# Performance work log

Measured on AMD Instinct MI355X. Metric: run time of the kernel, lower is better.

The kernel has to match this reference:

```python
import jax, jax.numpy as jnp
import numpy as np

N_ATOM, N_BOND, N_MOL, D = 250000, 250000, 10000, 64
BN_EPS = 1e-5


def _bn(x, gamma, beta):
    # torch BatchNorm1d training-mode math (biased variance)
    m = jnp.mean(x, axis=0)
    v = jnp.var(x, axis=0)
    return (x - m) * jax.lax.rsqrt(v + BN_EPS) * gamma + beta


def setup_inputs() -> dict:
    key = jax.random.key(0)
    ks = jax.random.split(key, 12)
    h = jax.random.normal(ks[0], (N_ATOM, D), jnp.float32)
    e = jax.random.normal(ks[1], (N_BOND, D), jnp.float32)
    u = jax.random.normal(ks[2], (N_MOL, D), jnp.float32)
    norm_atom = jax.random.uniform(ks[3], (N_ATOM, 1), jnp.float32)
    norm_bond = jax.random.uniform(ks[4], (N_BOND, 1), jnp.float32)
    bond_u = jax.random.randint(ks[5], (N_BOND,), 0, N_ATOM, jnp.int32)
    bond_v = jax.random.randint(ks[6], (N_BOND,), 0, N_ATOM, jnp.int32)
    atom2mol = jax.random.randint(ks[7], (N_ATOM,), 0, N_MOL, jnp.int32)
    bond2mol = jax.random.randint(ks[8], (N_BOND,), 0, N_MOL, jnp.int32)
    # 9 Linear layers A..I stacked: order A,B,C,D,E,F,G,H,I
    Ws = jax.random.normal(ks[9], (9, D, D), jnp.float32) * 0.05
    bs = jax.random.normal(ks[10], (9, D), jnp.float32) * 0.05
    bn_gamma = jnp.ones((3, D), jnp.float32)   # [e, h, u]
    bn_beta = jnp.zeros((3, D), jnp.float32)
    return dict(h=h, e=e, u=u, norm_atom=norm_atom, norm_bond=norm_bond,
                Ws=Ws, bs=bs, bn_gamma=bn_gamma, bn_beta=bn_beta,
                bond_u=bond_u, bond_v=bond_v, atom2mol=atom2mol, bond2mol=bond2mol)


def reference(h, e, u, norm_atom, norm_bond, Ws, bs, bn_gamma, bn_beta,
              bond_u, bond_v, atom2mol, bond2mol):
    lin = lambda x, i: x @ Ws[i] + bs[i]
    Ah, Dh, Eh = lin(h, 0), lin(h, 3), lin(h, 4)
    Be = lin(e, 1)
    Cu, Fu = lin(u, 2), lin(u, 5)

    # bond update: a2b (sum of Ah of both endpoints) + b2b self-loop + g2b broadcast
    e_new = Ah[bond_u] + Ah[bond_v] + Be + Cu[bond2mol]
    e_new = e_new * norm_bond                  # graph_norm
    e_new = _bn(e_new, bn_gamma[0], bn_beta[0])
    e_new = jax.nn.elu(e_new)

    # atom update: a2a self-loop + gated b2a (select_not_equal == other endpoint's Eh) + g2a
    sig = jax.nn.sigmoid(e_new)                # [N_BOND, D]
    dst = jnp.concatenate([bond_u, bond_v])    # each bond sends to both endpoints
    Eh_other = jnp.concatenate([Eh[bond_v], Eh[bond_u]])
    sig2 = jnp.concatenate([sig, sig])
    num = jax.ops.segment_sum(sig2 * Eh_other, dst, num_segments=N_ATOM)
    den = jax.ops.segment_sum(sig2, dst, num_segments=N_ATOM) + 1e-6
    h_new = Dh + num / den + Fu[atom2mol]
    h_new = h_new * norm_atom                  # graph_norm
    h_new = _bn(h_new, bn_gamma[1], bn_beta[1])
    h_new = jax.nn.elu(h_new)

    # global update: mean(Gh over atoms) + mean(He over bonds) + g2g self-loop Iu
    Gh, He, Iu = lin(h_new, 6), lin(e_new, 7), lin(u, 8)
    cnt_a = jax.ops.segment_sum(jnp.ones((N_ATOM, 1), h.dtype), atom2mol, num_segments=N_MOL)
    cnt_b = jax.ops.segment_sum(jnp.ones((N_BOND, 1), e.dtype), bond2mol, num_segments=N_MOL)
    u_new = (jax.ops.segment_sum(Gh, atom2mol, num_segments=N_MOL) / jnp.maximum(cnt_a, 1.0)
             + jax.ops.segment_sum(He, bond2mol, num_segments=N_MOL) / jnp.maximum(cnt_b, 1.0)
             + Iu)
    u_new = _bn(u_new, bn_gamma[2], bn_beta[2])
    u_new = jax.nn.elu(u_new)

    return h_new, e_new, u_new
```

## Files before the change

### kernel.cpp

```cpp
#include <hip/hip_runtime.h>
#include <cmath>

#define DD 64
#define TILE 64
#define BLK 256

__device__ __forceinline__ float elu_f(float x) {
  return x > 0.f ? x : expm1f(x);
}

__device__ __forceinline__ void fma4(float4& a, float s, const float4 b) {
  a.x = fmaf(s, b.x, a.x);
  a.y = fmaf(s, b.y, a.y);
  a.z = fmaf(s, b.z, a.z);
  a.w = fmaf(s, b.w, a.w);
}
__device__ __forceinline__ void add4(float4& a, const float4 b) {
  a.x += b.x; a.y += b.y; a.z += b.z; a.w += b.w;
}
__device__ __forceinline__ void sqacc4(float4& a, const float4 b) {
  a.x = fmaf(b.x, b.x, a.x);
  a.y = fmaf(b.y, b.y, a.y);
  a.z = fmaf(b.z, b.z, a.z);
  a.w = fmaf(b.w, b.w, a.w);
}
__device__ __forceinline__ void scale4(float4& a, float s) {
  a.x *= s; a.y *= s; a.z *= s; a.w *= s;
}

__device__ __forceinline__ void matmul_tile(const float (*xs)[DD + 4], const float (*wl)[DD],
                                            int r0, int c0, float4 acc[4]) {
#pragma unroll 2
  for (int k0 = 0; k0 < DD; k0 += 4) {
    float4 x0 = *(const float4*)&xs[r0 + 0][k0];
    float4 x1 = *(const float4*)&xs[r0 + 1][k0];
    float4 x2 = *(const float4*)&xs[r0 + 2][k0];
    float4 x3 = *(const float4*)&xs[r0 + 3][k0];
    float4 w0 = *(const float4*)&wl[k0 + 0][c0];
    float4 w1 = *(const float4*)&wl[k0 + 1][c0];
    float4 w2 = *(const float4*)&wl[k0 + 2][c0];
    float4 w3 = *(const float4*)&wl[k0 + 3][c0];
    fma4(acc[0], x0.x, w0); fma4(acc[0], x0.y, w1); fma4(acc[0], x0.z, w2); fma4(acc[0], x0.w, w3);
    fma4(acc[1], x1.x, w0); fma4(acc[1], x1.y, w1); fma4(acc[1], x1.z, w2); fma4(acc[1], x1.w, w3);
    fma4(acc[2], x2.x, w0); fma4(acc[2], x2.y, w1); fma4(acc[2], x2.z, w2); fma4(acc[2], x2.w, w3);
    fma4(acc[3], x3.x, w0); fma4(acc[3], x3.y, w1); fma4(acc[3], x3.z, w2); fma4(acc[3], x3.w, w3);
  }
}

__global__ void cnt_kernel(const int* __restrict__ a2m, int na,
                           const int* __restrict__ b2m, int nb,
                           const int* __restrict__ bu, const int* __restrict__ bv,
                           int* __restrict__ cnta_i, int* __restrict__ cntb_i,
                           int* __restrict__ deg) {
  int i = blockIdx.x * blockDim.x + threadIdx.x;
  if (i < na) {
    atomicAdd(&cnta_i[a2m[i]], 1);
  } else if (i < na + nb) {
    int b = i - na;
    atomicAdd(&cntb_i[b2m[b]], 1);
    atomicAdd(&deg[bu[b]], 1);
    atomicAdd(&deg[bv[b]], 1);
  }
}

__global__ void seg_alloc_kernel(const int* __restrict__ deg, int n,
                                 int* __restrict__ start, int* __restrict__ gcount) {
  int i = blockIdx.x * blockDim.x + threadIdx.x;
  int lane = threadIdx.x & 63;
  int d = (i < n) ? deg[i] : 0;
  int pre = d;
#pragma unroll
  for (int off = 1; off < 64; off <<= 1) {
    int t = __shfl_up(pre, off, 64);
    if (lane >= off) pre += t;
  }
  int total = __shfl(pre, 63, 64);
  int excl = pre - d;
  int base = 0;
  if (lane == 63) base = atomicAdd(gcount, total);
  base = __shfl(base, 63, 64);
  if (i < n) start[i] = base + excl;
}

__global__ void fill_kernel(const int* __restrict__ bu, const int* __restrict__ bv, int nb,
                            const int* __restrict__ start, int* __restrict__ cur,
                            int2* __restrict__ adj) {
  int b = blockIdx.x * blockDim.x + threadIdx.x;
  if (b < nb) {
    int a0 = bu[b], a1 = bv[b];
    int p = start[a0] + atomicAdd(&cur[a0], 1);
    adj[p] = make_int2(b, a1);
    int q = start[a1] + atomicAdd(&cur[a1], 1);
    adj[q] = make_int2(b, a0);
  }
}

__global__ void fill_mol_kernel(const int* __restrict__ a2m, int na,
                                const int* __restrict__ b2m, int nb,
                                const int* __restrict__ start_ma, int* __restrict__ cur_ma,
                                int* __restrict__ lista,
                                const int* __restrict__ start_mb, int* __restrict__ cur_mb,
                                int* __restrict__ listb) {
  int i = blockIdx.x * blockDim.x + threadIdx.x;
  if (i < na) {
    int m = a2m[i];
    lista[start_ma[m] + atomicAdd(&cur_ma[m], 1)] = i;
  } else if (i < na + nb) {
    int b = i - na;
    int m = b2m[b];
    listb[start_mb[m] + atomicAdd(&cur_mb[m], 1)] = b;
  }
}

__global__ __launch_bounds__(BLK) void lin2_kernel(
    const float* __restrict__ x, int nrows,
    const float* __restrict__ W0, const float* __restrict__ b0, float* __restrict__ out0,
    const float* __restrict__ W1, const float* __restrict__ b1, float* __restrict__ out1) {
  __shared__ __align__(16) float xs[TILE][DD + 4];
  __shared__ __align__(16) float w0[DD][DD];
  __shared__ __align__(16) float w1[DD][DD];
  const int tid = threadIdx.x;
  const int base = blockIdx.x * TILE;
  int rows = nrows - base; if (rows > TILE) rows = TILE;
  for (int l = tid; l < DD * DD; l += BLK) {
    int r = l >> 6, c = l & 63;
    xs[r][c] = (r < rows) ? x[(size_t)(base + r) * DD + c] : 0.f;
    w0[r][c] = W0[l];
    w1[r][c] = W1[l];
  }
  __syncthreads();
  const int tr = tid >> 4, tc = tid & 15;
  const int r0 = tr * 4, c0 = tc * 4;
  float4 accA[4], accB[4];
#pragma unroll
  for (int i = 0; i < 4; ++i) {
    accA[i] = make_float4(0.f, 0.f, 0.f, 0.f);
    accB[i] = make_float4(0.f, 0.f, 0.f, 0.f);
  }
#pragma unroll 1
  for (int k0 = 0; k0 < DD; k0 += 4) {
    float4 x0 = *(const float4*)&xs[r0 + 0][k0];
    float4 x1 = *(const float4*)&xs[r0 + 1][k0];
    float4 x2 = *(const float4*)&xs[r0 + 2][k0];
    float4 x3 = *(const float4*)&xs[r0 + 3][k0];
    float4 wa0 = *(const float4*)&w0[k0 + 0][c0];
    float4 wa1 = *(const float4*)&w0[k0 + 1][c0];
    float4 wa2 = *(const float4*)&w0[k0 + 2][c0];
    float4 wa3 = *(const float4*)&w0[k0 + 3][c0];
    float4 wb0 = *(const float4*)&w1[k0 + 0][c0];
    float4 wb1 = *(const float4*)&w1[k0 + 1][c0];
    float4 wb2 = *(const float4*)&w1[k0 + 2][c0];
    float4 wb3 = *(const float4*)&w1[k0 + 3][c0];
    fma4(accA[0], x0.x, wa0); fma4(accA[0], x0.y, wa1); fma4(accA[0], x0.z, wa2); fma4(accA[0], x0.w, wa3);
    fma4(accA[1], x1.x, wa0); fma4(accA[1], x1.y, wa1); fma4(accA[1], x1.z, wa2); fma4(accA[1], x1.w, wa3);
    fma4(accA[2], x2.x, wa0); fma4(accA[2], x2.y, wa1); fma4(accA[2], x2.z, wa2); fma4(accA[2], x2.w, wa3);
    fma4(accA[3], x3.x, wa0); fma4(accA[3], x3.y, wa1); fma4(accA[3], x3.z, wa2); fma4(accA[3], x3.w, wa3);
    fma4(accB[0], x0.x, wb0); fma4(accB[0], x0.y, wb1); fma4(accB[0], x0.z, wb2); fma4(accB[0], x0.w, wb3);
    fma4(accB[1], x1.x, wb0); fma4(accB[1], x1.y, wb1); fma4(accB[1], x1.z, wb2); fma4(accB[1], x1.w, wb3);
    fma4(accB[2], x2.x, wb0); fma4(accB[2], x2.y, wb1); fma4(accB[2], x2.z, wb2); fma4(accB[2], x2.w, wb3);
    fma4(accB[3], x3.x, wb0); fma4(accB[3], x3.y, wb1); fma4(accB[3], x3.z, wb2); fma4(accB[3], x3.w, wb3);
  }
  float4 bv0 = *(const float4*)&b0[c0];
  float4 bv1 = *(const float4*)&b1[c0];
#pragma unroll
  for (int i = 0; i < 4; ++i) {
    if (r0 + i < rows) {
      size_t rb = (size_t)(base + r0 + i) * DD + c0;
      float4 o0 = accA[i]; add4(o0, bv0);
      float4 o1 = accB[i]; add4(o1, bv1);
      *(float4*)&out0[rb] = o0;
      *(float4*)&out1[rb] = o1;
    }
  }
}

__global__ __launch_bounds__(BLK) void bond1_kernel(
    const float* __restrict__ e, int nrows, int ntiles,
    const float* __restrict__ W1, const float* __restrict__ b1,
    const float* __restrict__ Ah, const float* __restrict__ Cu,
    const int* __restrict__ bu, const int* __restrict__ bv, const int* __restrict__ b2m,
    const float* __restrict__ nrm,
    float* __restrict__ e_pre,
    float* __restrict__ ssum, float* __restrict__ ssq) {
  __shared__ __align__(16) float xs[TILE][DD + 4];
  __shared__ __align__(16) float wl[DD][DD];
  __shared__ int sbu[TILE], sbv[TILE], sbm[TILE];
  __shared__ float snb[TILE];
  __shared__ __align__(16) float red[16][DD];
  const int tid = threadIdx.x;
  const int tr = tid >> 4, tc = tid & 15, r0 = tr * 4, c0 = tc * 4;
  for (int l = tid; l < DD * DD; l += BLK) wl[l >> 6][l & 63] = W1[l];
  float4 bp = *(const float4*)&b1[c0];
  float4 lsum = make_float4(0.f, 0.f, 0.f, 0.f);
  float4 lsq  = make_float4(0.f, 0.f, 0.f, 0.f);
  for (int tile = blockIdx.x; tile < ntiles; tile += gridDim.x) {
    const int base = tile * TILE;
    int rows = nrows - base; if (rows > TILE) rows = TILE;
    __syncthreads();
    for (int l = tid; l < TILE * DD; l += BLK) {
      int r = l >> 6, c = l & 63;
      xs[r][c] = (r < rows) ? e[(size_t)(base + r) * DD + c] : 0.f;
    }
    if (tid < TILE) {
      bool v = tid < rows;
      int rb = base + tid;
      sbu[tid] = v ? bu[rb] : 0;
      sbv[tid] = v ? bv[rb] : 0;
      sbm[tid] = v ? b2m[rb] : 0;
      snb[tid] = v ? nrm[rb] : 0.f;
    }
    __syncthreads();
    float4 acc[4];
#pragma unroll
    for (int i = 0; i < 4; ++i) acc[i] = make_float4(0.f, 0.f, 0.f, 0.f);
    matmul_tile(xs, wl, r0, c0, acc);
#pragma unroll
    for (int i = 0; i < 4; ++i) {
      int r = r0 + i;
      if (r < rows) {
        int rb = base + r;
        float nb = snb[r];
        float4 ga = *(const float4*)&Ah[(size_t)sbu[r] * DD + c0];
        float4 gb = *(const float4*)&Ah[(size_t)sbv[r] * DD + c0];
        float4 gc = *(const float4*)&Cu[(size_t)sbm[r] * DD + c0];
        float4 o = acc[i];
        add4(o, bp); add4(o, ga); add4(o, gb); add4(o, gc);
        scale4(o, nb);
        add4(lsum, o); sqacc4(lsq, o);
        *(float4*)&e_pre[(size_t)rb * DD + c0] = o;
      }
    }
  }
  __syncthreads();
  *(float4*)&red[tr][c0] = lsum;
  __syncthreads();
  if (tid < DD) {
    float s = 0.f;
#pragma unroll
    for (int t = 0; t < 16; ++t) s += red[t][tid];
    atomicAdd(&ssum[tid], s);
  }
  __syncthreads();
  *(float4*)&red[tr][c0] = lsq;
  __syncthreads();
  if (tid < DD) {
    float s = 0.f;
#pragma unroll
    for (int t = 0; t < 16; ++t) s += red[t][tid];
    atomicAdd(&ssq[tid], s);
  }
}

__global__ void bnfinal_kernel(const float* __restrict__ ssum, const float* __restrict__ ssq,
                               const float* __restrict__ gamma, const float* __restrict__ beta,
                               float invN, float* __restrict__ scale, float* __restrict__ shift) {
  int j = threadIdx.x;
  float m = ssum[j] * invN;
  float v = ssq[j] * invN - m * m;
  float sc = gamma[j] * rsqrtf(v + 1e-5f);
  scale[j] = sc;
  shift[j] = beta[j] - m * sc;
}

__global__ void bn_elu_vec_kernel(float* __restrict__ x, long n4,
                                  const float* __restrict__ scale,
                                  const float* __restrict__ shift) {
  long stride = (long)gridDim.x * blockDim.x;
  for (long i = blockIdx.x * (long)blockDim.x + threadIdx.x; i < n4; i += stride) {
    float4 v = ((float4*)x)[i];
    int c0 = (int)((i & 15) << 2);
    float4 sc = *(const float4*)&scale[c0];
    float4 sh = *(const float4*)&shift[c0];
    v.x = elu_f(fmaf(v.x, sc.x, sh.x));
    v.y = elu_f(fmaf(v.y, sc.y, sh.y));
    v.z = elu_f(fmaf(v.z, sc.z, sh.z));
    v.w = elu_f(fmaf(v.w, sc.w, sh.w));
    ((float4*)x)[i] = v;
  }
}

__global__ __launch_bounds__(BLK) void agg_kernel(
    const float* __restrict__ e_act, const float* __restrict__ Eh,
    const int* __restrict__ start, const int* __restrict__ deg,
    const int2* __restrict__ adj, int na,
    float* __restrict__ aggout) {
  int wid = (int)((blockIdx.x * (unsigned)blockDim.x + threadIdx.x) >> 6);
  int lane = threadIdx.x & 63;
  if (wid >= na) return;
  int s = start[wid], d = deg[wid];
  float num = 0.f, den = 0.f;
  for (int k = 0; k < d; ++k) {
    int2 ent = adj[s + k];
    float ev = e_act[(size_t)ent.x * DD + lane];
    float sg = 1.f / (1.f + expf(-ev));
    float eh = Eh[(size_t)ent.y * DD + lane];
    num = fmaf(sg, eh, num);
    den += sg;
  }
  aggout[(size_t)wid * DD + lane] = num / (den + 1e-6f);
}

__global__ __launch_bounds__(BLK) void molsum_kernel(
    const float* __restrict__ src, const int* __restrict__ start,
    const int* __restrict__ cnt, const int* __restrict__ list, int nm,
    float* __restrict__ out) {
  int wid = (int)((blockIdx.x * (unsigned)blockDim.x + threadIdx.x) >> 6);
  int lane = threadIdx.x & 63;
  if (wid >= nm) return;
  int s = start[wid], c = cnt[wid];
  float acc = 0.f;
  for (int k = 0; k < c; ++k) {
    acc += src[(size_t)list[s + k] * DD + lane];
  }
  out[(size_t)wid * DD + lane] = acc;
}

__global__ __launch_bounds__(BLK) void atom1_kernel(
    const float* __restrict__ h, int nrows, int ntiles,
    const float* __restrict__ W3, const float* __restrict__ b3,
    const float* __restrict__ Fu,
    const int* __restrict__ a2m, const float* __restrict__ nrm,
    float* __restrict__ hio,
    float* __restrict__ ssum, float* __restrict__ ssq) {
  __shared__ __align__(16) float xs[TILE][DD + 4];
  __shared__ __align__(16) float wl[DD][DD];
  __shared__ int sam[TILE];
  __shared__ float sna[TILE];
  __shared__ __align__(16) float red[16][DD];
  const int tid = threadIdx.x;
  const int tr = tid >> 4, tc = tid & 15, r0 = tr * 4, c0 = tc * 4;
  for (int l = tid; l < DD * DD; l += BLK) wl[l >> 6][l & 63] = W3[l];
  float4 bp = *(const float4*)&b3[c0];
  float4 lsum = make_float4(0.f, 0.f, 0.f, 0.f);
  float4 lsq  = make_float4(0.f, 0.f, 0.f, 0.f);
  for (int tile = blockIdx.x; tile < ntiles; tile += gridDim.x) {
    const int base = tile * TILE;
    int rows = nrows - base; if (rows > TILE) rows = TILE;
    __syncthreads();
    for (int l = tid; l < TILE * DD; l += BLK) {
      int r = l >> 6, c = l & 63;
      xs[r][c] = (r < rows) ? h[(size_t)(base + r) * DD + c] : 0.f;
    }
    if (tid < TILE) {
      bool v = tid < rows;
      int rb = base + tid;
      sam[tid] = v ? a2m[rb] : 0;
      sna[tid] = v ? nrm[rb] : 0.f;
    }
    __syncthreads();
    float4 acc[4];
#pragma unroll
    for (int i = 0; i < 4; ++i) acc[i] = make_float4(0.f, 0.f, 0.f, 0.f);
    matmul_tile(xs, wl, r0, c0, acc);
#pragma unroll
    for (int i = 0; i < 4; ++i) {
      int r = r0 + i;
      if (r < rows) {
        size_t rb = (size_t)(base + r) * DD + c0;
        float na = sna[r];
        float4 g4 = *(const float4*)&hio[rb];
        float4 f4 = *(const float4*)&Fu[(size_t)sam[r] * DD + c0];
        float4 o;
        o.x = (acc[i].x + bp.x + g4.x + f4.x) * na;
        o.y = (acc[i].y + bp.y + g4.y + f4.y) * na;
        o.z = (acc[i].z + bp.z + g4.z + f4.z) * na;
        o.w = (acc[i].w + bp.w + g4.w + f4.w) * na;
        add4(lsum, o); sqacc4(lsq, o);
        *(float4*)&hio[rb] = o;
      }
    }
  }
  __syncthreads();
  *(float4*)&red[tr][c0] = lsum;
  __syncthreads();
  if (tid < DD) {
    float s = 0.f;
#pragma unroll
    for (int t = 0; t < 16; ++t) s += red[t][tid];
    atomicAdd(&ssum[tid], s);
  }
  __syncthreads();
  *(float4*)&red[tr][c0] = lsq;
  __syncthreads();
  if (tid < DD) {
    float s = 0.f;
#pragma unroll
    for (int t = 0; t < 16; ++t) s += red[t][tid];
    atomicAdd(&ssq[tid], s);
  }
}

__global__ __launch_bounds__(BLK) void global1_kernel(
    const float* __restrict__ u, int nrows,
    const float* __restrict__ W6, const float* __restrict__ W7, const float* __restrict__ W8,
    const float* __restrict__ b6, const float* __restrict__ b7, const float* __restrict__ b8,
    const float* __restrict__ msa, const float* __restrict__ msb,
    const int* __restrict__ cnta, const int* __restrict__ cntb,
    float* __restrict__ upre,
    float* __restrict__ ssum, float* __restrict__ ssq) {
  __shared__ __align__(16) float xsu[TILE][DD + 4];
  __shared__ __align__(16) float xsa[TILE][DD + 4];
  __shared__ __align__(16) float xsb[TILE][DD + 4];
  __shared__ __align__(16) float w6s[DD][DD];
  __shared__ __align__(16) float w7s[DD][DD];
  __shared__ __align__(16) float w8s[DD][DD];
  __shared__ float sfa[TILE], sfb[TILE];
  __shared__ __align__(16) float red[16][DD];
  const int tid = threadIdx.x;
  const int base = blockIdx.x * TILE;
  int rows = nrows - base; if (rows > TILE) rows = TILE;
  for (int l = tid; l < DD * DD; l += BLK) {
    int r = l >> 6, c = l & 63;
    w6s[r][c] = W6[l];
    w7s[r][c] = W7[l];
    w8s[r][c] = W8[l];
  }
  for (int l = tid; l < TILE * DD; l += BLK) {
    int r = l >> 6, c = l & 63;
    bool v = r < rows;
    float ca = 1.f, cb = 1.f;
    if (v) {
      int ia = cnta[base + r], ib = cntb[base + r];
      ca = ia > 0 ? (float)ia : 1.f;
      cb = ib > 0 ? (float)ib : 1.f;
    }
    xsu[r][c] = v ? u[(size_t)(base + r) * DD + c] : 0.f;
    xsa[r][c] = v ? msa[(size_t)(base + r) * DD + c] / ca : 0.f;
    xsb[r][c] = v ? msb[(size_t)(base + r) * DD + c] / cb : 0.f;
  }
  if (tid < TILE) {
    bool v = tid < rows;
    sfa[tid] = (v && cnta[base + tid] > 0) ? 1.f : 0.f;
    sfb[tid] = (v && cntb[base + tid] > 0) ? 1.f : 0.f;
  }
  __syncthreads();
  const int tr = tid >> 4, tc = tid & 15, r0 = tr * 4, c0 = tc * 4;
  float4 acc[4];
#pragma unroll
  for (int i = 0; i < 4; ++i) acc[i] = make_float4(0.f, 0.f, 0.f, 0.f);
  matmul_tile(xsu, w8s, r0, c0, acc);
  matmul_tile(xsa, w6s, r0, c0, acc);
  matmul_tile(xsb, w7s, r0, c0, acc);
  float4 b6v = *(const float4*)&b6[c0];
  float4 b7v = *(const float4*)&b7[c0];
  float4 b8v = *(const float4*)&b8[c0];
  float4 lsum = make_float4(0.f, 0.f, 0.f, 0.f);
  float4 lsq  = make_float4(0.f, 0.f, 0.f, 0.f);
#pragma unroll
  for (int i = 0; i < 4; ++i) {
    int r = r0 + i;
    if (r < rows) {
      size_t rb = (size_t)(base + r) * DD + c0;
      float fa = sfa[r], fb = sfb[r];
      float4 o = acc[i];
      o.x += b8v.x + fa * b6v.x + fb * b7v.x;
      o.y += b8v.y + fa * b6v.y + fb * b7v.y;
      o.z += b8v.z + fa * b6v.z + fb * b7v.z;
      o.w += b8v.w + fa * b6v.w + fb * b7v.w;
      add4(lsum, o); sqacc4(lsq, o);
      *(float4*)&upre[rb] = o;
    }
  }
  __syncthreads();
  *(float4*)&red[tr][c0] = lsum;
  __syncthreads();
  if (tid < DD) {
    float s = 0.f;
#pragma unroll
    for (int t = 0; t < 16; ++t) s += red[t][tid];
    atomicAdd(&ssum[tid], s);
  }
  __syncthreads();
  *(float4*)&red[tr][c0] = lsq;
  __syncthreads();
  if (tid < DD) {
    float s = 0.f;
#pragma unroll
    for (int t = 0; t < 16; ++t) s += red[t][tid];
    atomicAdd(&ssq[tid], s);
  }
}

extern "C" void kernel_launch(void* const* d_in, const int* in_sizes, int n_in,
                              void* d_out, int out_size, void* d_ws, size_t ws_size,
                              hipStream_t stream) {
  const float* h         = (const float*)d_in[0];
  const float* e         = (const float*)d_in[1];
  const float* u         = (const float*)d_in[2];
  const float* norm_atom = (const float*)d_in[3];
  const float* norm_bond = (const float*)d_in[4];
  const float* Ws        = (const float*)d_in[5];
  const float* bsarr     = (const float*)d_in[6];
  const float* bn_gamma  = (const float*)d_in[7];
  const float* bn_beta   = (const float*)d_in[8];
  const int* bond_u      = (const int*)d_in[9];
  const int* bond_v      = (const int*)d_in[10];
  const int* a2m         = (const int*)d_in[11];
  const int* b2m         = (const int*)d_in[12];

  const int NA = in_sizes[0] / DD;
  const int NB = in_sizes[1] / DD;
  const int NM = in_sizes[2] / DD;

  float* out_h = (float*)d_out;
  float* out_e = out_h + (size_t)NA * DD;
  float* out_u = out_e + (size_t)NB * DD;

  float* f     = (float*)d_ws;
  float* Ah    = f;
  float* Eh    = Ah + (size_t)NA * DD;
  float* Cu    = Eh + (size_t)NA * DD;
  float* Fu    = Cu + (size_t)NM * DD;
  float* msa   = Fu + (size_t)NM * DD;
  float* msb   = msa + (size_t)NM * DD;
  float* stats = msb + (size_t)NM * DD;
  float* sum_e = stats, *sq_e = stats + 64;
  float* sum_h = stats + 128, *sq_h = stats + 192;
  float* sum_u = stats + 256, *sq_u = stats + 320;
  int* deg     = (int*)(stats + 384);
  int* cur     = deg + NA;
  int* cnta_i  = cur + NA;
  int* cntb_i  = cnta_i + NM;
  int* cur_ma  = cntb_i + NM;
  int* cur_mb  = cur_ma + NM;
  int* gcounts = cur_mb + NM;
  float* bnp   = (float*)(gcounts + 4);
  float* sc_e = bnp, *sh_e = bnp + 64;
  float* sc_h = bnp + 128, *sh_h = bnp + 192;
  float* sc_u = bnp + 256, *sh_u = bnp + 320;
  int* start    = (int*)(bnp + 384);
  int* start_ma = start + NA;
  int* start_mb = start_ma + NM;
  int* lista    = start_mb + NM;
  int* listb    = lista + NA;
  int2* adj     = (int2*)(listb + NB);

  const float* W0 = Ws + 0 * 4096; const float* b0 = bsarr + 0 * 64;
  const float* W1 = Ws + 1 * 4096; const float* b1 = bsarr + 1 * 64;
  const float* W2 = Ws + 2 * 4096; const float* b2 = bsarr + 2 * 64;
  const float* W3 = Ws + 3 * 4096; const float* b3 = bsarr + 3 * 64;
  const float* W4 = Ws + 4 * 4096; const float* b4 = bsarr + 4 * 64;
  const float* W5 = Ws + 5 * 4096; const float* b5 = bsarr + 5 * 64;
  const float* W6 = Ws + 6 * 4096; const float* b6 = bsarr + 6 * 64;
  const float* W7 = Ws + 7 * 4096; const float* b7 = bsarr + 7 * 64;
  const float* W8 = Ws + 8 * 4096; const float* b8 = bsarr + 8 * 64;

  const int tiles_a = (NA + TILE - 1) / TILE;
  const int tiles_b = (NB + TILE - 1) / TILE;
  const int tiles_m = (NM + TILE - 1) / TILE;

  size_t zbytes = 384 * sizeof(float) + ((size_t)NA * 2 + (size_t)NM * 4 + 4) * sizeof(int);
  hipMemsetAsync(stats, 0, zbytes, stream);

  cnt_kernel<<<(NA + NB + BLK - 1) / BLK, BLK, 0, stream>>>(a2m, NA, b2m, NB,
                                                            bond_u, bond_v,
                                                            cnta_i, cntb_i, deg);
  seg_alloc_kernel<<<(NA + BLK - 1) / BLK, BLK, 0, stream>>>(deg, NA, start, gcounts + 0);
  seg_alloc_kernel<<<(NM + BLK - 1) / BLK, BLK, 0, stream>>>(cnta_i, NM, start_ma, gcounts + 1);
  seg_alloc_kernel<<<(NM + BLK - 1) / BLK, BLK, 0, stream>>>(cntb_i, NM, start_mb, gcounts + 2);
  fill_kernel<<<(NB + BLK - 1) / BLK, BLK, 0, stream>>>(bond_u, bond_v, NB, start, cur, adj);
  fill_mol_kernel<<<(NA + NB + BLK - 1) / BLK, BLK, 0, stream>>>(a2m, NA, b2m, NB,
                                                                 start_ma, cur_ma, lista,
                                                                 start_mb, cur_mb, listb);

  lin2_kernel<<<tiles_a, BLK, 0, stream>>>(h, NA, W0, b0, Ah, W4, b4, Eh);
  lin2_kernel<<<tiles_m, BLK, 0, stream>>>(u, NM, W2, b2, Cu, W5, b5, Fu);

  int nblk_b = tiles_b < 2048 ? tiles_b : 2048;
  bond1_kernel<<<nblk_b, BLK, 0, stream>>>(e, NB, tiles_b, W1, b1, Ah, Cu,
                                           bond_u, bond_v, b2m, norm_bond,
                                           out_e, sum_e, sq_e);
  bnfinal_kernel<<<1, 64, 0, stream>>>(sum_e, sq_e, bn_gamma + 0, bn_beta + 0,
                                       1.f / (float)NB, sc_e, sh_e);

  {
    long n4 = (long)NB * (DD / 4);
    int blocks = (int)((n4 + BLK - 1) / BLK); if (blocks > 2048) blocks = 2048;
    bn_elu_vec_kernel<<<blocks, BLK, 0, stream>>>(out_e, n4, sc_e, sh_e);
  }

  agg_kernel<<<(NA + 3) / 4, BLK, 0, stream>>>(out_e, Eh, start, deg, adj, NA, out_h);

  int nblk_a = tiles_a < 2048 ? tiles_a : 2048;
  atom1_kernel<<<nblk_a, BLK, 0, stream>>>(h, NA, tiles_a, W3, b3, Fu,
                                           a2m, norm_atom, out_h, sum_h, sq_h);
  bnfinal_kernel<<<1, 64, 0, stream>>>(sum_h, sq_h, bn_gamma + 64, bn_beta + 64,
                                       1.f / (float)NA, sc_h, sh_h);

  {
    long n4 = (long)NA * (DD / 4);
    int blocks = (int)((n4 + BLK - 1) / BLK); if (blocks > 2048) blocks = 2048;
    bn_elu_vec_kernel<<<blocks, BLK, 0, stream>>>(out_h, n4, sc_h, sh_h);
  }

  molsum_kernel<<<(NM + 3) / 4, BLK, 0, stream>>>(out_h, start_ma, cnta_i, lista, NM, msa);
  molsum_kernel<<<(NM + 3) / 4, BLK, 0, stream>>>(out_e, start_mb, cntb_i, listb, NM, msb);

  global1_kernel<<<tiles_m, BLK, 0, stream>>>(u, NM, W6, W7, W8, b6, b7, b8,
                                              msa, msb, cnta_i, cntb_i,
                                              out_u, sum_u, sq_u);
  bnfinal_kernel<<<1, 64, 0, stream>>>(sum_u, sq_u, bn_gamma + 128, bn_beta + 128,
                                       1.f / (float)NM, sc_u, sh_u);
  {
    long n4 = (long)NM * (DD / 4);
    int blocks = (int)((n4 + BLK - 1) / BLK); if (blocks > 2048) blocks = 2048;
    bn_elu_vec_kernel<<<blocks, BLK, 0, stream>>>(out_u, n4, sc_u, sh_u);
  }
}
```

Before: 743.0 us.

## Fuse atom epilogue and BN stats into gather aggregation, precompute Dh

Measured after the change: 779.1 us. 4.9% more time.

```diff
diff --git a/kernel.cpp b/kernel.cpp
--- a/kernel.cpp
+++ b/kernel.cpp
@@ -7,6 +7,9 @@
 
 __device__ __forceinline__ float elu_f(float x) {
   return x > 0.f ? x : expm1f(x);
+}
+__device__ __forceinline__ float sigmoid_fast(float x) {
+  return __builtin_amdgcn_rcpf(1.f + __expf(-x));
 }
 
 __device__ __forceinline__ void fma4(float4& a, float s, const float4 b) {
@@ -170,6 +173,37 @@
       float4 o1 = accB[i]; add4(o1, bv1);
       *(float4*)&out0[rb] = o0;
       *(float4*)&out1[rb] = o1;
+    }
+  }
+}
+
+__global__ __launch_bounds__(BLK) void lin1_kernel(
+    const float* __restrict__ x, int nrows,
+    const float* __restrict__ W, const float* __restrict__ b, float* __restrict__ out) {
+  __shared__ __align__(16) float xs[TILE][DD + 4];
+  __shared__ __align__(16) float wl[DD][DD];
+  const int tid = threadIdx.x;
+  const int base = blockIdx.x * TILE;
+  int rows = nrows - base; if (rows > TILE) rows = TILE;
+  for (int l = tid; l < DD * DD; l += BLK) {
+    int r = l >> 6, c = l & 63;
+    xs[r][c] = (r < rows) ? x[(size_t)(base + r) * DD + c] : 0.f;
+    wl[r][c] = W[l];
+  }
+  __syncthreads();
+  const int tr = tid >> 4, tc = tid & 15;
+  const int r0 = tr * 4, c0 = tc * 4;
+  float4 acc[4];
+#pragma unroll
+  for (int i = 0; i < 4; ++i) acc[i] = make_float4(0.f, 0.f, 0.f, 0.f);
+  matmul_tile(xs, wl, r0, c0, acc);
+  float4 bv = *(const float4*)&b[c0];
+#pragma unroll
+  for (int i = 0; i < 4; ++i) {
+    if (r0 + i < rows) {
+      size_t rb = (size_t)(base + r0 + i) * DD + c0;
+      float4 o = acc[i]; add4(o, bv);
+      *(float4*)&out[rb] = o;
     }
   }
 }
@@ -279,25 +313,64 @@
   }
 }
 
-__global__ __launch_bounds__(BLK) void agg_kernel(
+__global__ __launch_bounds__(BLK) void agg_fused_kernel(
     const float* __restrict__ e_act, const float* __restrict__ Eh,
+    const float* __restrict__ Dhb, const float* __restrict__ Fu,
+    const int* __restrict__ a2m, const float* __restrict__ nrm,
     const int* __restrict__ start, const int* __restrict__ deg,
     const int2* __restrict__ adj, int na,
-    float* __restrict__ aggout) {
-  int wid = (int)((blockIdx.x * (unsigned)blockDim.x + threadIdx.x) >> 6);
-  int lane = threadIdx.x & 63;
-  if (wid >= na) return;
-  int s = start[wid], d = deg[wid];
-  float num = 0.f, den = 0.f;
-  for (int k = 0; k < d; ++k) {
-    int2 ent = adj[s + k];
-    float ev = e_act[(size_t)ent.x * DD + lane];
-    float sg = 1.f / (1.f + expf(-ev));
-    float eh = Eh[(size_t)ent.y * DD + lane];
-    num = fmaf(sg, eh, num);
-    den += sg;
-  }
-  aggout[(size_t)wid * DD + lane] = num / (den + 1e-6f);
+    float* __restrict__ hpre,
+    float* __restrict__ ssum, float* __restrict__ ssq) {
+  const int tid = threadIdx.x;
+  const int lane = tid & 63;
+  const int wv = tid >> 6;
+  const int wstep = (gridDim.x * BLK) >> 6;
+  float lsum = 0.f, lsq = 0.f;
+  for (int wid = blockIdx.x * (BLK >> 6) + wv; wid < na; wid += wstep) {
+    float dh = Dhb[(size_t)wid * DD + lane];
+    float fu = Fu[(size_t)a2m[wid] * DD + lane];
+    float nr = nrm[wid];
+    int s = start[wid], d = deg[wid];
+    float num = 0.f, den = 0.f;
+    int k = 0;
+    for (; k + 2 <= d; k += 2) {
+      int2 e0 = adj[s + k];
+      int2 e1 = adj[s + k + 1];
+      float ev0 = e_act[(size_t)e0.x * DD + lane];
+      float eh0 = Eh[(size_t)e0.y * DD + lane];
+      float ev1 = e_act[(size_t)e1.x * DD + lane];
+      float eh1 = Eh[(size_t)e1.y * DD + lane];
+      float sg0 = sigmoid_fast(ev0);
+      float sg1 = sigmoid_fast(ev1);
+      num = fmaf(sg0, eh0, num); den += sg0;
+      num = fmaf(sg1, eh1, num); den += sg1;
+    }
+    if (k < d) {
+      int2 e0 = adj[s + k];
+      float ev0 = e_act[(size_t)e0.x * DD + lane];
+      float eh0 = Eh[(size_t)e0.y * DD + lane];
+      float sg0 = sigmoid_fast(ev0);
+      num = fmaf(sg0, eh0, num); den += sg0;
+    }
+    float o = (dh + num / (den + 1e-6f) + fu) * nr;
+    hpre[(size_t)wid * DD + lane] = o;
+    lsum += o;
+    lsq = fmaf(o, o, lsq);
+  }
+  __shared__ __align__(16) float red[BLK / 64][DD];
+  red[wv][lane] = lsum;
+  __syncthreads();
+  if (tid < DD) {
+    float s4 = red[0][tid] + red[1][tid] + red[2][tid] + red[3][tid];
+    atomicAdd(&ssum[tid], s4);
+  }
+  __syncthreads();
+  red[wv][lane] = lsq;
+  __syncthreads();
+  if (tid < DD) {
+    float s4 = red[0][tid] + red[1][tid] + red[2][tid] + red[3][tid];
+    atomicAdd(&ssq[tid], s4);
+  }
 }
 
 __global__ __launch_bounds__(BLK) void molsum_kernel(
@@ -309,85 +382,15 @@
   if (wid >= nm) return;
   int s = start[wid], c = cnt[wid];
   float acc = 0.f;
-  for (int k = 0; k < c; ++k) {
-    acc += src[(size_t)list[s + k] * DD + lane];
-  }
+  int k = 0;
+  for (; k + 2 <= c; k += 2) {
+    int i0 = list[s + k], i1 = list[s + k + 1];
+    float v0 = src[(size_t)i0 * DD + lane];
+    float v1 = src[(size_t)i1 * DD + lane];
+    acc += v0 + v1;
+  }
+  if (k < c) acc += src[(size_t)list[s + k] * DD + lane];
   out[(size_t)wid * DD + lane] = acc;
-}
-
-__global__ __launch_bounds__(BLK) void atom1_kernel(
-    const float* __restrict__ h, int nrows, int ntiles,
-    const float* __restrict__ W3, const float* __restrict__ b3,
-    const float* __restrict__ Fu,
-    const int* __restrict__ a2m, const float* __restrict__ nrm,
-    float* __restrict__ hio,
-    float* __restrict__ ssum, float* __restrict__ ssq) {
-  __shared__ __align__(16) float xs[TILE][DD + 4];
-  __shared__ __align__(16) float wl[DD][DD];
-  __shared__ int sam[TILE];
-  __shared__ float sna[TILE];
-  __shared__ __align__(16) float red[16][DD];
-  const int tid = threadIdx.x;
-  const int tr = tid >> 4, tc = tid & 15, r0 = tr * 4, c0 = tc * 4;
-  for (int l = tid; l < DD * DD; l += BLK) wl[l >> 6][l & 63] = W3[l];
-  float4 bp = *(const float4*)&b3[c0];
-  float4 lsum = make_float4(0.f, 0.f, 0.f, 0.f);
-  float4 lsq  = make_float4(0.f, 0.f, 0.f, 0.f);
-  for (int tile = blockIdx.x; tile < ntiles; tile += gridDim.x) {
-    const int base = tile * TILE;
-    int rows = nrows - base; if (rows > TILE) rows = TILE;
-    __syncthreads();
-    for (int l = tid; l < TILE * DD; l += BLK) {
-      int r = l >> 6, c = l & 63;
-      xs[r][c] = (r < rows) ? h[(size_t)(base + r) * DD + c] : 0.f;
-    }
-    if (tid < TILE) {
-      bool v = tid < rows;
-      int rb = base + tid;
-      sam[tid] = v ? a2m[rb] : 0;
-      sna[tid] = v ? nrm[rb] : 0.f;
-    }
-    __syncthreads();
-    float4 acc[4];
-#pragma unroll
-    for (int i = 0; i < 4; ++i) acc[i] = make_float4(0.f, 0.f, 0.f, 0.f);
-    matmul_tile(xs, wl, r0, c0, acc);
-#pragma unroll
-    for (int i = 0; i < 4; ++i) {
-      int r = r0 + i;
-      if (r < rows) {
-        size_t rb = (size_t)(base + r) * DD + c0;
-        float na = sna[r];
-        float4 g4 = *(const float4*)&hio[rb];
-        float4 f4 = *(const float4*)&Fu[(size_t)sam[r] * DD + c0];
-        float4 o;
-        o.x = (acc[i].x + bp.x + g4.x + f4.x) * na;
-        o.y = (acc[i].y + bp.y + g4.y + f4.y) * na;
-        o.z = (acc[i].z + bp.z + g4.z + f4.z) * na;
-        o.w = (acc[i].w + bp.w + g4.w + f4.w) * na;
-        add4(lsum, o); sqacc4(lsq, o);
-        *(float4*)&hio[rb] = o;
-      }
-    }
-  }
-  __syncthreads();
-  *(float4*)&red[tr][c0] = lsum;
-  __syncthreads();
-  if (tid < DD) {
-    float s = 0.f;
-#pragma unroll
-    for (int t = 0; t < 16; ++t) s += red[t][tid];
-    atomicAdd(&ssum[tid], s);
-  }
-  __syncthreads();
-  *(float4*)&red[tr][c0] = lsq;
-  __syncthreads();
-  if (tid < DD) {
-    float s = 0.f;
-#pragma unroll
-    for (int t = 0; t < 16; ++t) s += red[t][tid];
-    atomicAdd(&ssq[tid], s);
-  }
 }
 
 __global__ __launch_bounds__(BLK) void global1_kernel(
@@ -508,6 +511,7 @@
 
   float* f     = (float*)d_ws;
   float* Ah    = f;
+  float* Dhb   = Ah;
   float* Eh    = Ah + (size_t)NA * DD;
   float* Cu    = Eh + (size_t)NA * DD;
   float* Fu    = Cu + (size_t)NM * DD;
@@ -579,11 +583,14 @@
     bn_elu_vec_kernel<<<blocks, BLK, 0, stream>>>(out_e, n4, sc_e, sh_e);
   }
 
-  agg_kernel<<<(NA + 3) / 4, BLK, 0, stream>>>(out_e, Eh, start, deg, adj, NA, out_h);
-
-  int nblk_a = tiles_a < 2048 ? tiles_a : 2048;
-  atom1_kernel<<<nblk_a, BLK, 0, stream>>>(h, NA, tiles_a, W3, b3, Fu,
-                                           a2m, norm_atom, out_h, sum_h, sq_h);
+  lin1_kernel<<<tiles_a, BLK, 0, stream>>>(h, NA, W3, b3, Dhb);
+
+  {
+    int blocks = (NA + 3) / 4; if (blocks > 8192) blocks = 8192;
+    agg_fused_kernel<<<blocks, BLK, 0, stream>>>(out_e, Eh, Dhb, Fu, a2m, norm_atom,
+                                                 start, deg, adj, NA,
+                                                 out_h, sum_h, sq_h);
+  }
   bnfinal_kernel<<<1, 64, 0, stream>>>(sum_h, sq_h, bn_gamma + 64, bn_beta + 64,
                                        1.f / (float)NA, sc_h, sh_h);
 
```
